# Performance work log

Measured on AMD Instinct MI355X. Metric: run time of the kernel, lower is better.

The kernel has to match this reference:

```python
import jax, jax.numpy as jnp
from jax import lax
import numpy as np

NUM_SCALES = 4
NUM_ORI = 8
SIGMA = 2.0
FILTER_SIZE = 32  # min(512 // 2**scale, 32) == 32 for all scales, already even
J = 4
POOL = 2 ** J  # 16


def _make_gabor_filters():
    """Replicates GaborWavelet2D + _init_wavelet_filters. Returns (real, imag) stacks
    of shape [num_scales*num_ori, 1, FILTER_SIZE, FILTER_SIZE]."""
    oris = np.linspace(0.0, np.pi, NUM_ORI)
    idx = np.arange(FILTER_SIZE, dtype=np.float32) - FILTER_SIZE // 2
    X, Y = np.meshgrid(idx, idx, indexing='ij')
    reals, imags = [], []
    for scale in range(1, NUM_SCALES + 1):
        for o in oris:
            Xr = X * np.cos(o) + Y * np.sin(o)
            Yr = -X * np.sin(o) + Y * np.cos(o)
            sf = scale * SIGMA
            env = np.exp(-0.5 * (Xr ** 2 + Yr ** 2) / sf ** 2)
            phase = 2.0 * np.pi * (1.0 / scale) * Xr / sf
            reals.append(env * np.cos(phase))
            imags.append(env * np.sin(phase))
    real = np.stack(reals).astype(np.float32)[:, None]  # [32,1,32,32]
    imag = np.stack(imags).astype(np.float32)[:, None]
    return real, imag


def setup_inputs() -> dict:
    key = jax.random.key(0)
    x = jax.random.normal(key, (8, 3, 512, 512), dtype=jnp.float32)
    w_real, w_imag = _make_gabor_filters()
    return {"x": x, "w_real": jnp.asarray(w_real), "w_imag": jnp.asarray(w_imag)}


def _avg_pool(t):
    # torch F.avg_pool2d(kernel=16), default stride=kernel, floor mode (drop remainder)
    B, C, H, W = t.shape
    Ho, Wo = H // POOL, W // POOL
    t = t[:, :, :Ho * POOL, :Wo * POOL]
    return t.reshape(B, C, Ho, POOL, Wo, POOL).mean(axis=(3, 5))


def reference(x, w_real, w_imag):
    # x: [B,3,512,512]
    x_gray = x.mean(axis=1, keepdims=True)  # [B,1,H,W]
    S0 = _avg_pool(x_gray)  # [B,1,32,32]

    pad = FILTER_SIZE // 2  # 16 -> conv output is (H+1, W+1) = 513x513
    w = jnp.concatenate([w_real, w_imag], axis=0)  # [64,1,32,32]
    conv = lax.conv_general_dilated(
        x_gray, w, window_strides=(1, 1), padding=((pad, pad), (pad, pad)),
        dimension_numbers=('NCHW', 'OIHW', 'NCHW'))  # [B,64,513,513], cross-correlation like torch
    nf = w_real.shape[0]
    cr, ci = conv[:, :nf], conv[:, nf:]
    mag = jnp.sqrt(cr ** 2 + ci ** 2 + 1e-8)  # [B,32,513,513]
    S1 = _avg_pool(mag)  # [B,32,32,32]
    return (S0, S1)
```

## Files before the change

### kernel.cpp

```cpp
#include <hip/hip_runtime.h>
#include <math.h>

#define IMG   512
#define NFILT 32
#define NPAIR 16
#define PI_F  3.14159265358979323846f
#define GS    104

typedef _Float16 v8h __attribute__((ext_vector_type(8)));
typedef float    v4f __attribute__((ext_vector_type(4)));

__device__ __forceinline__ unsigned pkrtz(float a, float b) {
    typedef __fp16 f16x2 __attribute__((ext_vector_type(2)));
    union { f16x2 h; unsigned u; } x;
    x.h = __builtin_amdgcn_cvt_pkrtz(a, b);
    return x.u;
}

template <int CTRL>
__device__ __forceinline__ float dpp_add(float v) {
    int t = __builtin_amdgcn_update_dpp(0, __float_as_int(v), CTRL, 0xf, 0xf, true);
    return v + __int_as_float(t);
}

__device__ __forceinline__ float xor32_add(float m) {
    float a = m, b = m;
    asm("v_permlane32_swap_b32 %0, %1" : "+v"(a), "+v"(b));
    return a + b;
}

#if __has_builtin(__builtin_amdgcn_sqrtf)
__device__ __forceinline__ float fsqrt(float x) { return __builtin_amdgcn_sqrtf(x); }
#else
__device__ __forceinline__ float fsqrt(float x) { return sqrtf(x); }
#endif

__device__ __forceinline__ void bar_lgkm() {
    asm volatile("s_waitcnt lgkmcnt(0)\n\ts_barrier" ::: "memory");
}

__device__ __forceinline__ v8h ldfrag(const uint4* p) {
    union { uint4 u; v8h h; } x; x.u = *p; return x.h;
}

__global__ void make_tables(unsigned* __restrict__ tabs) {
    __shared__ _Float16 P[5][168];
    const int fo = blockIdx.x;
    const int tid = threadIdx.x;
    for (int e = tid; e < 5 * 168; e += 256) ((_Float16*)P)[e] = (_Float16)0.0f;
    __syncthreads();
    if (tid < 160) {
        int tbl = tid >> 5, t = tid & 31;
        int s = (fo >> 3) + 1, o = fo & 7;
        float theta = (float)o * (PI_F / 7.0f);
        float sf = (float)s * 2.0f;
        float kf = 2.0f * PI_F / ((float)s * sf);
        float a = kf * cosf(theta), b = kf * sinf(theta);
        float d = (float)(t - 16);
        float env = expf(-0.5f * d * d / (sf * sf));
        float v;
        switch (tbl) {
            case 0: v =  env * cosf(b * d); break;
            case 1: v =  env * sinf(b * d); break;
            case 2: v =  env * cosf(a * d); break;
            case 3: v =  env * sinf(a * d); break;
            default: v = -env * sinf(a * d); break;
        }
        P[tbl][t + 64] = (_Float16)v;
    }
    __syncthreads();
    unsigned* dst = tabs + (size_t)fo * 3200;
    for (int e = tid; e < 3200; e += 256) {
        int tbl  = e / 640;  int rem2 = e - tbl * 640;
        int copy = rem2 / 80; int idw = rem2 - copy * 80;
        int p0 = (idw >> 2) * 8 + copy + (idw & 3) * 2;
        union { unsigned u; _Float16 h[2]; } p;
        p.h[0] = P[tbl][p0];
        p.h[1] = P[tbl][p0 + 1];
        dst[e] = p.u;
    }
}

__launch_bounds__(512, 4)
__global__ void conv_kernel(const float* __restrict__ x,
                            const uint4* __restrict__ tabs,
                            float* __restrict__ s0out,
                            float* __restrict__ s1out) {
    __shared__ _Float16 gray[96 * GS];
    __shared__ _Float16 Tre[2][64 * GS];
    __shared__ _Float16 Tim[2][64 * GS];
    __shared__ float    s1st[NFILT * 16];

    const int bx = blockIdx.x;
    const int n  = bx >> 6;
    const int t6 = bx & 63;
    const int ty = t6 >> 3, tx = t6 & 7;
    const int r0g = ty * 64 - 16;
    const int c0g = tx * 64 - 16;
    const int tid = threadIdx.x;

    const int lane = tid & 63;
    const int w    = tid >> 6;
    const int r4   = w & 3;
    const int half = w >> 2;
    const int nn   = lane & 15;
    const int q8   = (lane >> 4) << 3;
    const int q4   = (lane >> 4) << 2;
    const int cr   = r4 * 16 + nn;
    const int u    = q8 - cr + 64;
    const int b0   = r4 >> 1;
    const int uoff = (u & 7) * 20 + (u >> 3);

    const uint4* fb0 = tabs + uoff;
    v8h Gre0[2], Gim0[2], Fre[2], Fim[2];
    #pragma unroll
    for (int j = 0; j < 2; ++j) {
        int idx = (b0 + j) * 4;
        Gre0[j] = ldfrag(fb0 + idx);
        Gim0[j] = ldfrag(fb0 + 160 + idx);
        Fre[j]  = ldfrag(fb0 + 320 + idx);
        Fim[j]  = ldfrag(fb0 + 480 + idx);
    }

    {
        const float* c0p = x + (size_t)n * 3 * IMG * IMG;
        const float* c1p = c0p + IMG * IMG;
        const float* c2p = c0p + 2 * IMG * IMG;
        for (int e = tid; e < 96 * 24; e += 512) {
            int hr = e / 24, g4 = e - hr * 24;
            int hc0 = g4 * 4;
            int gr = r0g + hr, gc0 = c0g + hc0;
            float4 v = make_float4(0.f, 0.f, 0.f, 0.f);
            if (hr < 95 && (unsigned)gr < IMG && (unsigned)gc0 < IMG) {
                size_t off = ((size_t)gr * IMG + gc0) >> 2;
                float4 a = ((const float4*)c0p)[off];
                float4 b = ((const float4*)c1p)[off];
                float4 c = ((const float4*)c2p)[off];
                v.x = (a.x + b.x + c.x) * (1.0f / 3.0f);
                v.y = (a.y + b.y + c.y) * (1.0f / 3.0f);
                v.z = (a.z + b.z + c.z) * (1.0f / 3.0f);
                v.w = (hc0 == 92) ? 0.0f : (a.w + b.w + c.w) * (1.0f / 3.0f);
            }
            uint2 w2;
            w2.x = pkrtz(v.x, v.y);
            w2.y = pkrtz(v.z, v.w);
            *(uint2*)(&gray[hr * GS + hc0]) = w2;
        }
    }
    __syncthreads();

    if (tid < 256) {
        int cell = tid >> 4, sub = tid & 15;
        int pr = cell >> 2, pc = cell & 3;
        const _Float16* row = &gray[(16 + pr * 16 + sub) * GS + 16 + pc * 16];
        float s = 0.0f;
        #pragma unroll
        for (int j = 0; j < 16; ++j) s += (float)row[j];
        s += __shfl_xor(s, 1);
        s += __shfl_xor(s, 2);
        s += __shfl_xor(s, 4);
        s += __shfl_xor(s, 8);
        if (sub == 0)
            s0out[(size_t)n * 1024 + (ty * 4 + pr) * 32 + (tx * 4 + pc)] = s * (1.0f / 256.0f);
    }


    v8h Agray[3][2];
    #pragma unroll
    for (int mi = 0; mi < 3; ++mi)
        #pragma unroll
        for (int j = 0; j < 2; ++j)
            Agray[mi][j] = *(const v8h*)(&gray[((half * 3 + mi) * 16 + nn) * GS + (b0 + j) * 32 + q8]);

    #pragma unroll
    for (int mi = 0; mi < 3; ++mi) {
        int mt = half * 3 + mi;
        v4f aR = {0.f, 0.f, 0.f, 0.f}, aI = {0.f, 0.f, 0.f, 0.f};
        #pragma unroll
        for (int j = 0; j < 2; ++j) {
            aR = __builtin_amdgcn_mfma_f32_16x16x32_f16(Agray[mi][j], Gre0[j], aR, 0, 0, 0);
            aI = __builtin_amdgcn_mfma_f32_16x16x32_f16(Agray[mi][j], Gim0[j], aI, 0, 0, 0);
        }
        int mb = mt * 16 + q4;
        uint2 pr, pi;
        pr.x = pkrtz(aR[0], aR[1]);  pr.y = pkrtz(aR[2], aR[3]);
        pi.x = pkrtz(aI[0], aI[1]);  pi.y = pkrtz(aI[2], aI[3]);
        *(uint2*)(&Tre[0][cr * GS + mb]) = pr;
        *(uint2*)(&Tim[0][cr * GS + mb]) = pi;
    }
    __syncthreads();

    for (int p = 0; p < NPAIR; ++p) {
        const _Float16* Tr  = Tre[p & 1];
        const _Float16* Ti  = Tim[p & 1];
        _Float16*       Trn = Tre[(p + 1) & 1];
        _Float16*       Tin = Tim[(p + 1) & 1];
        const int fa  = ((p >> 2) << 3) + (p & 3);
        const int fbi = ((p >> 2) << 3) + 7 - (p & 3);
        const int nxp = (p < NPAIR - 1) ? p + 1 : p;
        const int nxfa = ((nxp >> 2) << 3) + (nxp & 3);
        const uint4* fbn = tabs + (size_t)nxfa * 800 + uoff;

        v8h Gre[2], Gim[2];
        #pragma unroll
        for (int j = 0; j < 2; ++j) {
            int idx = (b0 + j) * 4;
            Gre[j] = ldfrag(fbn + idx);
            Gim[j] = ldfrag(fbn + 160 + idx);
        }

        #pragma unroll
        for (int ni = 0; ni < 2; ++ni) {
            int nt = half * 2 + ni;
            v4f P1 = {0.f, 0.f, 0.f, 0.f}, P2 = {0.f, 0.f, 0.f, 0.f};
            v4f P3 = {0.f, 0.f, 0.f, 0.f}, P4 = {0.f, 0.f, 0.f, 0.f};
            #pragma unroll
            for (int j = 0; j < 2; ++j) {
                v8h tR = *(const v8h*)(&Tr[(nt * 16 + nn) * GS + (b0 + j) * 32 + q8]);
                v8h tI = *(const v8h*)(&Ti[(nt * 16 + nn) * GS + (b0 + j) * 32 + q8]);
                P1 = __builtin_amdgcn_mfma_f32_16x16x32_f16(Fre[j], tR, P1, 0, 0, 0);
                P2 = __builtin_amdgcn_mfma_f32_16x16x32_f16(Fim[j], tI, P2, 0, 0, 0);
                P3 = __builtin_amdgcn_mfma_f32_16x16x32_f16(Fre[j], tI, P3, 0, 0, 0);
                P4 = __builtin_amdgcn_mfma_f32_16x16x32_f16(Fim[j], tR, P4, 0, 0, 0);
            }
            v4f are = P1 - P2, aim = P3 + P4;
            v4f bre = P1 + P2, bim = P3 - P4;
            float sa0 = fsqrt(fmaf(are[0], are[0], fmaf(aim[0], aim[0], 1e-8f)));
            float sa1 = fsqrt(fmaf(are[1], are[1], fmaf(aim[1], aim[1], 1e-8f)));
            float sa2 = fsqrt(fmaf(are[2], are[2], fmaf(aim[2], aim[2], 1e-8f)));
            float sa3 = fsqrt(fmaf(are[3], are[3], fmaf(aim[3], aim[3], 1e-8f)));
            float sb0 = fsqrt(fmaf(bre[0], bre[0], fmaf(bim[0], bim[0], 1e-8f)));
            float sb1 = fsqrt(fmaf(bre[1], bre[1], fmaf(bim[1], bim[1], 1e-8f)));
            float sb2 = fsqrt(fmaf(bre[2], bre[2], fmaf(bim[2], bim[2], 1e-8f)));
            float sb3 = fsqrt(fmaf(bre[3], bre[3], fmaf(bim[3], bim[3], 1e-8f)));
            float ma = (sa0 + sa1) + (sa2 + sa3);
            float mb = (sb0 + sb1) + (sb2 + sb3);
            ma = dpp_add<0xB1>(ma);   mb = dpp_add<0xB1>(mb);
            ma = dpp_add<0x4E>(ma);   mb = dpp_add<0x4E>(mb);
            ma = dpp_add<0x141>(ma);  mb = dpp_add<0x141>(mb);
            ma = dpp_add<0x140>(ma);  mb = dpp_add<0x140>(mb);
            ma += __shfl_xor(ma, 16); mb += __shfl_xor(mb, 16);
            ma = xor32_add(ma);       mb = xor32_add(mb);
            if (lane == 0) {
                s1st[fa  * 16 + r4 * 4 + nt] = ma;
                s1st[fbi * 16 + r4 * 4 + nt] = mb;
            }
        }

        if (p < NPAIR - 1) {
            #pragma unroll
            for (int mi = 0; mi < 3; ++mi) {
                int mt = half * 3 + mi;
                v4f aR = {0.f, 0.f, 0.f, 0.f}, aI = {0.f, 0.f, 0.f, 0.f};
                #pragma unroll
                for (int j = 0; j < 2; ++j) {
                    aR = __builtin_amdgcn_mfma_f32_16x16x32_f16(Agray[mi][j], Gre[j], aR, 0, 0, 0);
                    aI = __builtin_amdgcn_mfma_f32_16x16x32_f16(Agray[mi][j], Gim[j], aI, 0, 0, 0);
                }
                int mb = mt * 16 + q4;
                uint2 pr, pi;
                pr.x = pkrtz(aR[0], aR[1]);  pr.y = pkrtz(aR[2], aR[3]);
                pi.x = pkrtz(aI[0], aI[1]);  pi.y = pkrtz(aI[2], aI[3]);
                *(uint2*)(&Trn[cr * GS + mb]) = pr;
                *(uint2*)(&Tin[cr * GS + mb]) = pi;
            }
            #pragma unroll
            for (int j = 0; j < 2; ++j) {
                int idx = (b0 + j) * 4;
                Fre[j] = ldfrag(fbn + 320 + idx);
                Fim[j] = ldfrag(fbn + 480 + idx);
            }
        }
        bar_lgkm();
    }

    float* s1b = s1out + (size_t)n * NFILT * 32 * 32;
    for (int e = tid; e < NFILT * 16; e += 512) {
        int fi = e >> 4, cell = e & 15;
        int r4c = cell >> 2, ntc = cell & 3;
        s1b[((size_t)fi * 32 + (ty * 4 + r4c)) * 32 + (tx * 4 + ntc)] =
            s1st[e] * (1.0f / 256.0f);
    }
}

extern "C" void kernel_launch(void* const* d_in, const int* in_sizes, int n_in,
                              void* d_out, int out_size, void* d_ws, size_t ws_size,
                              hipStream_t stream) {
    const float* x = (const float*)d_in[0];
    float* out = (float*)d_out;
    unsigned* tabs = (unsigned*)d_ws;

    hipLaunchKernelGGL(make_tables, dim3(32), dim3(256), 0, stream, tabs);
    hipLaunchKernelGGL(conv_kernel, dim3(512), dim3(512), 0, stream,
                       x, (const uint4*)tabs, out, out + 8192);
}
```

Measured before the change: 113.3 us.

## Software-pipeline magnitude reduction one pair behind MFMA accumulation

Defers the sqrt and wavefront-reduction epilogue for each filter pair to the next loop iteration, so it interleaves with that iteration's MFMA work. Both column tiles' accumulators are computed together, and s_setprio raises wave priority around the matrix-core section. The cross-lane swap is replaced by a generic shuffle xor 32. This holds more accumulators live, which raises register pressure and adds an extra epilogue and barrier after the loop. The final deferred reduction uses filter indices 27 and 28, which matches p=15.

```diff
diff --git a/kernel.cpp b/kernel.cpp
--- a/kernel.cpp
+++ b/kernel.cpp
@@ -23,11 +23,6 @@
     return v + __int_as_float(t);
 }
 
-__device__ __forceinline__ float xor32_add(float m) {
-    float a = m, b = m;
-    asm("v_permlane32_swap_b32 %0, %1" : "+v"(a), "+v"(b));
-    return a + b;
-}
 
 #if __has_builtin(__builtin_amdgcn_sqrtf)
 __device__ __forceinline__ float fsqrt(float x) { return __builtin_amdgcn_sqrtf(x); }
@@ -164,7 +159,6 @@
             s0out[(size_t)n * 1024 + (ty * 4 + pr) * 32 + (tx * 4 + pc)] = s * (1.0f / 256.0f);
     }
 
-
     v8h Agray[3][2];
     #pragma unroll
     for (int mi = 0; mi < 3; ++mi)
@@ -190,60 +184,80 @@
     }
     __syncthreads();
 
+    auto magred = [&](v4f P1, v4f P2, v4f P3, v4f P4, int faI, int fbI, int ntc) {
+        v4f are = P1 - P2, aim = P3 + P4;
+        v4f bre = P1 + P2, bim = P3 - P4;
+        float sa0 = fsqrt(fmaf(are[0], are[0], fmaf(aim[0], aim[0], 1e-8f)));
+        float sa1 = fsqrt(fmaf(are[1], are[1], fmaf(aim[1], aim[1], 1e-8f)));
+        float sa2 = fsqrt(fmaf(are[2], are[2], fmaf(aim[2], aim[2], 1e-8f)));
+        float sa3 = fsqrt(fmaf(are[3], are[3], fmaf(aim[3], aim[3], 1e-8f)));
+        float sb0 = fsqrt(fmaf(bre[0], bre[0], fmaf(bim[0], bim[0], 1e-8f)));
+        float sb1 = fsqrt(fmaf(bre[1], bre[1], fmaf(bim[1], bim[1], 1e-8f)));
+        float sb2 = fsqrt(fmaf(bre[2], bre[2], fmaf(bim[2], bim[2], 1e-8f)));
+        float sb3 = fsqrt(fmaf(bre[3], bre[3], fmaf(bim[3], bim[3], 1e-8f)));
+        float ma = (sa0 + sa1) + (sa2 + sa3);
+        float mb = (sb0 + sb1) + (sb2 + sb3);
+        ma = dpp_add<0xB1>(ma);   mb = dpp_add<0xB1>(mb);
+        ma = dpp_add<0x4E>(ma);   mb = dpp_add<0x4E>(mb);
+        ma = dpp_add<0x141>(ma);  mb = dpp_add<0x141>(mb);
+        ma = dpp_add<0x140>(ma);  mb = dpp_add<0x140>(mb);
+        ma += __shfl_xor(ma, 16); mb += __shfl_xor(mb, 16);
+        ma += __shfl_xor(ma, 32); mb += __shfl_xor(mb, 32);
+        if (lane == 0) {
+            s1st[faI * 16 + r4 * 4 + ntc] = ma;
+            s1st[fbI * 16 + r4 * 4 + ntc] = mb;
+        }
+    };
+
+    v4f P1a = {0,0,0,0}, P2a = {0,0,0,0}, P3a = {0,0,0,0}, P4a = {0,0,0,0};
+    v4f P1b = {0,0,0,0}, P2b = {0,0,0,0}, P3b = {0,0,0,0}, P4b = {0,0,0,0};
+
     for (int p = 0; p < NPAIR; ++p) {
         const _Float16* Tr  = Tre[p & 1];
         const _Float16* Ti  = Tim[p & 1];
         _Float16*       Trn = Tre[(p + 1) & 1];
         _Float16*       Tin = Tim[(p + 1) & 1];
-        const int fa  = ((p >> 2) << 3) + (p & 3);
-        const int fbi = ((p >> 2) << 3) + 7 - (p & 3);
-        const int nxp = (p < NPAIR - 1) ? p + 1 : p;
+        const int nxp  = (p < NPAIR - 1) ? p + 1 : p;
         const int nxfa = ((nxp >> 2) << 3) + (nxp & 3);
         const uint4* fbn = tabs + (size_t)nxfa * 800 + uoff;
 
         v8h Gre[2], Gim[2];
-        #pragma unroll
-        for (int j = 0; j < 2; ++j) {
-            int idx = (b0 + j) * 4;
-            Gre[j] = ldfrag(fbn + idx);
-            Gim[j] = ldfrag(fbn + 160 + idx);
-        }
-
-        #pragma unroll
-        for (int ni = 0; ni < 2; ++ni) {
-            int nt = half * 2 + ni;
-            v4f P1 = {0.f, 0.f, 0.f, 0.f}, P2 = {0.f, 0.f, 0.f, 0.f};
-            v4f P3 = {0.f, 0.f, 0.f, 0.f}, P4 = {0.f, 0.f, 0.f, 0.f};
+        if (p < NPAIR - 1) {
             #pragma unroll
             for (int j = 0; j < 2; ++j) {
-                v8h tR = *(const v8h*)(&Tr[(nt * 16 + nn) * GS + (b0 + j) * 32 + q8]);
-                v8h tI = *(const v8h*)(&Ti[(nt * 16 + nn) * GS + (b0 + j) * 32 + q8]);
-                P1 = __builtin_amdgcn_mfma_f32_16x16x32_f16(Fre[j], tR, P1, 0, 0, 0);
-                P2 = __builtin_amdgcn_mfma_f32_16x16x32_f16(Fim[j], tI, P2, 0, 0, 0);
-                P3 = __builtin_amdgcn_mfma_f32_16x16x32_f16(Fre[j], tI, P3, 0, 0, 0);
-                P4 = __builtin_amdgcn_mfma_f32_16x16x32_f16(Fim[j], tR, P4, 0, 0, 0);
-            }
-            v4f are = P1 - P2, aim = P3 + P4;
-            v4f bre = P1 + P2, bim = P3 - P4;
-            float sa0 = fsqrt(fmaf(are[0], are[0], fmaf(aim[0], aim[0], 1e-8f)));
-            float sa1 = fsqrt(fmaf(are[1], are[1], fmaf(aim[1], aim[1], 1e-8f)));
-            float sa2 = fsqrt(fmaf(are[2], are[2], fmaf(aim[2], aim[2], 1e-8f)));
-            float sa3 = fsqrt(fmaf(are[3], are[3], fmaf(aim[3], aim[3], 1e-8f)));
-            float sb0 = fsqrt(fmaf(bre[0], bre[0], fmaf(bim[0], bim[0], 1e-8f)));
-            float sb1 = fsqrt(fmaf(bre[1], bre[1], fmaf(bim[1], bim[1], 1e-8f)));
-            float sb2 = fsqrt(fmaf(bre[2], bre[2], fmaf(bim[2], bim[2], 1e-8f)));
-            float sb3 = fsqrt(fmaf(bre[3], bre[3], fmaf(bim[3], bim[3], 1e-8f)));
-            float ma = (sa0 + sa1) + (sa2 + sa3);
-            float mb = (sb0 + sb1) + (sb2 + sb3);
-            ma = dpp_add<0xB1>(ma);   mb = dpp_add<0xB1>(mb);
-            ma = dpp_add<0x4E>(ma);   mb = dpp_add<0x4E>(mb);
-            ma = dpp_add<0x141>(ma);  mb = dpp_add<0x141>(mb);
-            ma = dpp_add<0x140>(ma);  mb = dpp_add<0x140>(mb);
-            ma += __shfl_xor(ma, 16); mb += __shfl_xor(mb, 16);
-            ma = xor32_add(ma);       mb = xor32_add(mb);
-            if (lane == 0) {
-                s1st[fa  * 16 + r4 * 4 + nt] = ma;
-                s1st[fbi * 16 + r4 * 4 + nt] = mb;
+                int idx = (b0 + j) * 4;
+                Gre[j] = ldfrag(fbn + idx);
+                Gim[j] = ldfrag(fbn + 160 + idx);
+            }
+        }
+
+        if (p > 0) {
+            const int q    = p - 1;
+            const int pfa  = ((q >> 2) << 3) + (q & 3);
+            const int pfbi = ((q >> 2) << 3) + 7 - (q & 3);
+            magred(P1a, P2a, P3a, P4a, pfa, pfbi, half * 2 + 0);
+            magred(P1b, P2b, P3b, P4b, pfa, pfbi, half * 2 + 1);
+        }
+
+        __builtin_amdgcn_s_setprio(1);
+        {
+            int nt0 = half * 2 + 0, nt1 = half * 2 + 1;
+            P1a = {0,0,0,0}; P2a = {0,0,0,0}; P3a = {0,0,0,0}; P4a = {0,0,0,0};
+            P1b = {0,0,0,0}; P2b = {0,0,0,0}; P3b = {0,0,0,0}; P4b = {0,0,0,0};
+            #pragma unroll
+            for (int j = 0; j < 2; ++j) {
+                v8h tR0 = *(const v8h*)(&Tr[(nt0 * 16 + nn) * GS + (b0 + j) * 32 + q8]);
+                v8h tI0 = *(const v8h*)(&Ti[(nt0 * 16 + nn) * GS + (b0 + j) * 32 + q8]);
+                v8h tR1 = *(const v8h*)(&Tr[(nt1 * 16 + nn) * GS + (b0 + j) * 32 + q8]);
+                v8h tI1 = *(const v8h*)(&Ti[(nt1 * 16 + nn) * GS + (b0 + j) * 32 + q8]);
+                P1a = __builtin_amdgcn_mfma_f32_16x16x32_f16(Fre[j], tR0, P1a, 0, 0, 0);
+                P2a = __builtin_amdgcn_mfma_f32_16x16x32_f16(Fim[j], tI0, P2a, 0, 0, 0);
+                P3a = __builtin_amdgcn_mfma_f32_16x16x32_f16(Fre[j], tI0, P3a, 0, 0, 0);
+                P4a = __builtin_amdgcn_mfma_f32_16x16x32_f16(Fim[j], tR0, P4a, 0, 0, 0);
+                P1b = __builtin_amdgcn_mfma_f32_16x16x32_f16(Fre[j], tR1, P1b, 0, 0, 0);
+                P2b = __builtin_amdgcn_mfma_f32_16x16x32_f16(Fim[j], tI1, P2b, 0, 0, 0);
+                P3b = __builtin_amdgcn_mfma_f32_16x16x32_f16(Fre[j], tI1, P3b, 0, 0, 0);
+                P4b = __builtin_amdgcn_mfma_f32_16x16x32_f16(Fim[j], tR1, P4b, 0, 0, 0);
             }
         }
 
@@ -264,15 +278,22 @@
                 *(uint2*)(&Trn[cr * GS + mb]) = pr;
                 *(uint2*)(&Tin[cr * GS + mb]) = pi;
             }
+            __builtin_amdgcn_s_setprio(0);
             #pragma unroll
             for (int j = 0; j < 2; ++j) {
                 int idx = (b0 + j) * 4;
                 Fre[j] = ldfrag(fbn + 320 + idx);
                 Fim[j] = ldfrag(fbn + 480 + idx);
             }
+        } else {
+            __builtin_amdgcn_s_setprio(0);
         }
         bar_lgkm();
     }
+
+    magred(P1a, P2a, P3a, P4a, 27, 28, half * 2 + 0);
+    magred(P1b, P2b, P3b, P4b, 27, 28, half * 2 + 1);
+    __syncthreads();
 
     float* s1b = s1out + (size_t)n * NFILT * 32 * 32;
     for (int e = tid; e < NFILT * 16; e += 512) {
```

Result: slower. 115.7 us (+2.1%).

## Keep separable-conv intermediate in registers, drop LDS double buffer and barriers

Applied to the files above, without the earlier changes.

Restructures the two-stage separable Gabor convolution so each wave computes its first-stage (row) MFMA output directly into register fragments. Those fragments are packed to fp16 and fed straight into 16x16x16 MFMAs for the second stage, removing the shared-memory T buffers, per-filter barriers and the staging array for S1. S1 results are written directly to global memory from each wave. The cost is redundant first-stage work: each wave recomputes the row convolution for its own tile, doubling those MFMAs, and filter fragments are reloaded from global memory every iteration.

```diff
diff --git a/kernel.cpp b/kernel.cpp
--- a/kernel.cpp
+++ b/kernel.cpp
@@ -8,7 +8,26 @@
 #define GS    104
 
 typedef _Float16 v8h __attribute__((ext_vector_type(8)));
+typedef _Float16 v4h __attribute__((ext_vector_type(4)));
 typedef float    v4f __attribute__((ext_vector_type(4)));
+
+#define MF32(a, b, c) __builtin_amdgcn_mfma_f32_16x16x32_f16((a), (b), (c), 0, 0, 0)
+
+#if __has_builtin(__builtin_amdgcn_mfma_f32_16x16x16f16)
+__device__ __forceinline__ v4f mf16(v4h a, v4h b, v4f c) {
+    return __builtin_amdgcn_mfma_f32_16x16x16f16(a, b, c, 0, 0, 0);
+}
+#elif __has_builtin(__builtin_amdgcn_mfma_f32_16x16x16_f16)
+__device__ __forceinline__ v4f mf16(v4h a, v4h b, v4f c) {
+    return __builtin_amdgcn_mfma_f32_16x16x16_f16(a, b, c, 0, 0, 0);
+}
+#else
+__device__ __forceinline__ v4f mf16(v4h a, v4h b, v4f c) {
+    asm("v_mfma_f32_16x16x16_f16 %0, %1, %2, %0" : "+v"(c) : "v"(a), "v"(b));
+    return c;
+}
+#endif
+#define MF16(a, b, c) mf16((a), (b), (c))
 
 __device__ __forceinline__ unsigned pkrtz(float a, float b) {
     typedef __fp16 f16x2 __attribute__((ext_vector_type(2)));
@@ -23,24 +42,23 @@
     return v + __int_as_float(t);
 }
 
-__device__ __forceinline__ float xor32_add(float m) {
-    float a = m, b = m;
-    asm("v_permlane32_swap_b32 %0, %1" : "+v"(a), "+v"(b));
-    return a + b;
-}
-
 #if __has_builtin(__builtin_amdgcn_sqrtf)
 __device__ __forceinline__ float fsqrt(float x) { return __builtin_amdgcn_sqrtf(x); }
 #else
 __device__ __forceinline__ float fsqrt(float x) { return sqrtf(x); }
 #endif
 
-__device__ __forceinline__ void bar_lgkm() {
-    asm volatile("s_waitcnt lgkmcnt(0)\n\ts_barrier" ::: "memory");
-}
-
 __device__ __forceinline__ v8h ldfrag(const uint4* p) {
     union { uint4 u; v8h h; } x; x.u = *p; return x.h;
+}
+__device__ __forceinline__ v4h ldfrag2(const uint2* p) {
+    union { uint2 u; v4h h; } x; x.u = *p; return x.h;
+}
+__device__ __forceinline__ v4h pk4(v4f a) {
+    union { unsigned u[2]; v4h h; } x;
+    x.u[0] = pkrtz(a[0], a[1]);
+    x.u[1] = pkrtz(a[2], a[3]);
+    return x.h;
 }
 
 __global__ void make_tables(unsigned* __restrict__ tabs) {
@@ -87,9 +105,6 @@
                             float* __restrict__ s0out,
                             float* __restrict__ s1out) {
     __shared__ _Float16 gray[96 * GS];
-    __shared__ _Float16 Tre[2][64 * GS];
-    __shared__ _Float16 Tim[2][64 * GS];
-    __shared__ float    s1st[NFILT * 16];
 
     const int bx = blockIdx.x;
     const int n  = bx >> 6;
@@ -102,25 +117,20 @@
     const int lane = tid & 63;
     const int w    = tid >> 6;
     const int r4   = w & 3;
-    const int half = w >> 2;
+    const int hh   = w >> 2;
     const int nn   = lane & 15;
     const int q8   = (lane >> 4) << 3;
     const int q4   = (lane >> 4) << 2;
-    const int cr   = r4 * 16 + nn;
-    const int u    = q8 - cr + 64;
     const int b0   = r4 >> 1;
-    const int uoff = (u & 7) * 20 + (u >> 3);
-
-    const uint4* fb0 = tabs + uoff;
-    v8h Gre0[2], Gim0[2], Fre[2], Fim[2];
-    #pragma unroll
-    for (int j = 0; j < 2; ++j) {
-        int idx = (b0 + j) * 4;
-        Gre0[j] = ldfrag(fb0 + idx);
-        Gim0[j] = ldfrag(fb0 + 160 + idx);
-        Fre[j]  = ldfrag(fb0 + 320 + idx);
-        Fim[j]  = ldfrag(fb0 + 480 + idx);
-    }
+
+    const int rr   = r4 * 16 + nn;
+    const int u0F  = q4 - rr + 64;
+    const int offF = (u0F & 7) * 20 + (u0F >> 3);
+    const int cG0  = 2 * hh * 16 + nn;
+    const int uG0  = q8 - cG0 + 64;
+    const int uG1  = uG0 - 16;
+    const int offG0 = (uG0 & 7) * 20 + (uG0 >> 3);
+    const int offG1 = (uG1 & 7) * 20 + (uG1 >> 3);
 
     {
         const float* c0p = x + (size_t)n * 3 * IMG * IMG;
@@ -164,122 +174,114 @@
             s0out[(size_t)n * 1024 + (ty * 4 + pr) * 32 + (tx * 4 + pc)] = s * (1.0f / 256.0f);
     }
 
-
-    v8h Agray[3][2];
+    v8h Agray[4][2];
     #pragma unroll
-    for (int mi = 0; mi < 3; ++mi)
-        #pragma unroll
-        for (int j = 0; j < 2; ++j)
-            Agray[mi][j] = *(const v8h*)(&gray[((half * 3 + mi) * 16 + nn) * GS + (b0 + j) * 32 + q8]);
-
-    #pragma unroll
-    for (int mi = 0; mi < 3; ++mi) {
-        int mt = half * 3 + mi;
-        v4f aR = {0.f, 0.f, 0.f, 0.f}, aI = {0.f, 0.f, 0.f, 0.f};
-        #pragma unroll
-        for (int j = 0; j < 2; ++j) {
-            aR = __builtin_amdgcn_mfma_f32_16x16x32_f16(Agray[mi][j], Gre0[j], aR, 0, 0, 0);
-            aI = __builtin_amdgcn_mfma_f32_16x16x32_f16(Agray[mi][j], Gim0[j], aI, 0, 0, 0);
-        }
-        int mb = mt * 16 + q4;
-        uint2 pr, pi;
-        pr.x = pkrtz(aR[0], aR[1]);  pr.y = pkrtz(aR[2], aR[3]);
-        pi.x = pkrtz(aI[0], aI[1]);  pi.y = pkrtz(aI[2], aI[3]);
-        *(uint2*)(&Tre[0][cr * GS + mb]) = pr;
-        *(uint2*)(&Tim[0][cr * GS + mb]) = pi;
-    }
-    __syncthreads();
+    for (int mi = 0; mi < 4; ++mi)
+        #pragma unroll
+        for (int jj = 0; jj < 2; ++jj)
+            Agray[mi][jj] = *(const v8h*)(&gray[((2 * b0 + mi) * 16 + nn) * GS + (hh + jj) * 32 + q8]);
+
+    float* s1b = s1out + (size_t)n * NFILT * 1024;
+
+    auto magstore = [&](v4f P1, v4f P2, v4f P3, v4f P4, int faI, int fbI, int ct) {
+        v4f are = P1 - P2, aim = P3 + P4;
+        v4f bre = P1 + P2, bim = P3 - P4;
+        float sa0 = fsqrt(fmaf(are[0], are[0], fmaf(aim[0], aim[0], 1e-8f)));
+        float sa1 = fsqrt(fmaf(are[1], are[1], fmaf(aim[1], aim[1], 1e-8f)));
+        float sa2 = fsqrt(fmaf(are[2], are[2], fmaf(aim[2], aim[2], 1e-8f)));
+        float sa3 = fsqrt(fmaf(are[3], are[3], fmaf(aim[3], aim[3], 1e-8f)));
+        float sb0 = fsqrt(fmaf(bre[0], bre[0], fmaf(bim[0], bim[0], 1e-8f)));
+        float sb1 = fsqrt(fmaf(bre[1], bre[1], fmaf(bim[1], bim[1], 1e-8f)));
+        float sb2 = fsqrt(fmaf(bre[2], bre[2], fmaf(bim[2], bim[2], 1e-8f)));
+        float sb3 = fsqrt(fmaf(bre[3], bre[3], fmaf(bim[3], bim[3], 1e-8f)));
+        float ma = (sa0 + sa1) + (sa2 + sa3);
+        float mb = (sb0 + sb1) + (sb2 + sb3);
+        ma = dpp_add<0xB1>(ma);   mb = dpp_add<0xB1>(mb);
+        ma = dpp_add<0x4E>(ma);   mb = dpp_add<0x4E>(mb);
+        ma = dpp_add<0x141>(ma);  mb = dpp_add<0x141>(mb);
+        ma = dpp_add<0x140>(ma);  mb = dpp_add<0x140>(mb);
+        ma += __shfl_xor(ma, 16); mb += __shfl_xor(mb, 16);
+        ma += __shfl_xor(ma, 32); mb += __shfl_xor(mb, 32);
+        if (lane == 0) {
+            s1b[((size_t)faI * 32 + (ty * 4 + r4)) * 32 + (tx * 4 + ct)] = ma * (1.0f / 256.0f);
+            s1b[((size_t)fbI * 32 + (ty * 4 + r4)) * 32 + (tx * 4 + ct)] = mb * (1.0f / 256.0f);
+        }
+    };
 
     for (int p = 0; p < NPAIR; ++p) {
-        const _Float16* Tr  = Tre[p & 1];
-        const _Float16* Ti  = Tim[p & 1];
-        _Float16*       Trn = Tre[(p + 1) & 1];
-        _Float16*       Tin = Tim[(p + 1) & 1];
         const int fa  = ((p >> 2) << 3) + (p & 3);
         const int fbi = ((p >> 2) << 3) + 7 - (p & 3);
-        const int nxp = (p < NPAIR - 1) ? p + 1 : p;
-        const int nxfa = ((nxp >> 2) << 3) + (nxp & 3);
-        const uint4* fbn = tabs + (size_t)nxfa * 800 + uoff;
-
-        v8h Gre[2], Gim[2];
-        #pragma unroll
-        for (int j = 0; j < 2; ++j) {
-            int idx = (b0 + j) * 4;
-            Gre[j] = ldfrag(fbn + idx);
-            Gim[j] = ldfrag(fbn + 160 + idx);
-        }
-
-        #pragma unroll
-        for (int ni = 0; ni < 2; ++ni) {
-            int nt = half * 2 + ni;
-            v4f P1 = {0.f, 0.f, 0.f, 0.f}, P2 = {0.f, 0.f, 0.f, 0.f};
-            v4f P3 = {0.f, 0.f, 0.f, 0.f}, P4 = {0.f, 0.f, 0.f, 0.f};
+        const uint4* ft  = tabs + (size_t)fa * 800;
+        const uint2* ft2 = (const uint2*)ft;
+
+        v4h Fr[4], Fi[4];
+        #pragma unroll
+        for (int s = 0; s < 4; ++s) {
+            Fr[s] = ldfrag2(ft2 + 640 + 2 * offF + 8 * b0 + 4 * s);
+            Fi[s] = ldfrag2(ft2 + 960 + 2 * offF + 8 * b0 + 4 * s);
+        }
+        v8h Gr[2], Gi[2];
+        #pragma unroll
+        for (int jj = 0; jj < 2; ++jj) {
+            Gr[jj] = ldfrag(ft + offG0 + (hh + jj) * 4);
+            Gi[jj] = ldfrag(ft + 160 + offG0 + (hh + jj) * 4);
+        }
+
+        v4h tre[4], tim[4];
+        #pragma unroll
+        for (int mi = 0; mi < 4; ++mi) {
+            v4f aR = {0.f, 0.f, 0.f, 0.f}, aI = {0.f, 0.f, 0.f, 0.f};
+            aR = MF32(Agray[mi][0], Gr[0], aR);
+            aI = MF32(Agray[mi][0], Gi[0], aI);
+            aR = MF32(Agray[mi][1], Gr[1], aR);
+            aI = MF32(Agray[mi][1], Gi[1], aI);
+            tre[mi] = pk4(aR);
+            tim[mi] = pk4(aI);
+        }
+
+        v8h Gr1[2], Gi1[2];
+        #pragma unroll
+        for (int jj = 0; jj < 2; ++jj) {
+            Gr1[jj] = ldfrag(ft + offG1 + (hh + jj) * 4);
+            Gi1[jj] = ldfrag(ft + 160 + offG1 + (hh + jj) * 4);
+        }
+
+        {
+            v4f P1 = {0.f,0.f,0.f,0.f}, P2 = {0.f,0.f,0.f,0.f};
+            v4f P3 = {0.f,0.f,0.f,0.f}, P4 = {0.f,0.f,0.f,0.f};
             #pragma unroll
-            for (int j = 0; j < 2; ++j) {
-                v8h tR = *(const v8h*)(&Tr[(nt * 16 + nn) * GS + (b0 + j) * 32 + q8]);
-                v8h tI = *(const v8h*)(&Ti[(nt * 16 + nn) * GS + (b0 + j) * 32 + q8]);
-                P1 = __builtin_amdgcn_mfma_f32_16x16x32_f16(Fre[j], tR, P1, 0, 0, 0);
-                P2 = __builtin_amdgcn_mfma_f32_16x16x32_f16(Fim[j], tI, P2, 0, 0, 0);
-                P3 = __builtin_amdgcn_mfma_f32_16x16x32_f16(Fre[j], tI, P3, 0, 0, 0);
-                P4 = __builtin_amdgcn_mfma_f32_16x16x32_f16(Fim[j], tR, P4, 0, 0, 0);
+            for (int s = 0; s < 4; ++s) {
+                P1 = MF16(Fr[s], tre[s], P1);
+                P2 = MF16(Fi[s], tim[s], P2);
+                P3 = MF16(Fr[s], tim[s], P3);
+                P4 = MF16(Fi[s], tre[s], P4);
             }
-            v4f are = P1 - P2, aim = P3 + P4;
-            v4f bre = P1 + P2, bim = P3 - P4;
-            float sa0 = fsqrt(fmaf(are[0], are[0], fmaf(aim[0], aim[0], 1e-8f)));
-            float sa1 = fsqrt(fmaf(are[1], are[1], fmaf(aim[1], aim[1], 1e-8f)));
-            float sa2 = fsqrt(fmaf(are[2], are[2], fmaf(aim[2], aim[2], 1e-8f)));
-            float sa3 = fsqrt(fmaf(are[3], are[3], fmaf(aim[3], aim[3], 1e-8f)));
-            float sb0 = fsqrt(fmaf(bre[0], bre[0], fmaf(bim[0], bim[0], 1e-8f)));
-            float sb1 = fsqrt(fmaf(bre[1], bre[1], fmaf(bim[1], bim[1], 1e-8f)));
-            float sb2 = fsqrt(fmaf(bre[2], bre[2], fmaf(bim[2], bim[2], 1e-8f)));
-            float sb3 = fsqrt(fmaf(bre[3], bre[3], fmaf(bim[3], bim[3], 1e-8f)));
-            float ma = (sa0 + sa1) + (sa2 + sa3);
-            float mb = (sb0 + sb1) + (sb2 + sb3);
-            ma = dpp_add<0xB1>(ma);   mb = dpp_add<0xB1>(mb);
-            ma = dpp_add<0x4E>(ma);   mb = dpp_add<0x4E>(mb);
-            ma = dpp_add<0x141>(ma);  mb = dpp_add<0x141>(mb);
-            ma = dpp_add<0x140>(ma);  mb = dpp_add<0x140>(mb);
-            ma += __shfl_xor(ma, 16); mb += __shfl_xor(mb, 16);
-            ma = xor32_add(ma);       mb = xor32_add(mb);
-            if (lane == 0) {
-                s1st[fa  * 16 + r4 * 4 + nt] = ma;
-                s1st[fbi * 16 + r4 * 4 + nt] = mb;
+            magstore(P1, P2, P3, P4, fa, fbi, 2 * hh);
+        }
+
+        #pragma unroll
+        for (int mi = 0; mi < 4; ++mi) {
+            v4f aR = {0.f, 0.f, 0.f, 0.f}, aI = {0.f, 0.f, 0.f, 0.f};
+            aR = MF32(Agray[mi][0], Gr1[0], aR);
+            aI = MF32(Agray[mi][0], Gi1[0], aI);
+            aR = MF32(Agray[mi][1], Gr1[1], aR);
+            aI = MF32(Agray[mi][1], Gi1[1], aI);
+            tre[mi] = pk4(aR);
+            tim[mi] = pk4(aI);
+        }
+
+        {
+            v4f P1 = {0.f,0.f,0.f,0.f}, P2 = {0.f,0.f,0.f,0.f};
+            v4f P3 = {0.f,0.f,0.f,0.f}, P4 = {0.f,0.f,0.f,0.f};
+            #pragma unroll
+            for (int s = 0; s < 4; ++s) {
+                P1 = MF16(Fr[s], tre[s], P1);
+                P2 = MF16(Fi[s], tim[s], P2);
+                P3 = MF16(Fr[s], tim[s], P3);
+                P4 = MF16(Fi[s], tre[s], P4);
             }
-        }
-
-        if (p < NPAIR - 1) {
-            #pragma unroll
-            for (int mi = 0; mi < 3; ++mi) {
-                int mt = half * 3 + mi;
-                v4f aR = {0.f, 0.f, 0.f, 0.f}, aI = {0.f, 0.f, 0.f, 0.f};
-                #pragma unroll
-                for (int j = 0; j < 2; ++j) {
-                    aR = __builtin_amdgcn_mfma_f32_16x16x32_f16(Agray[mi][j], Gre[j], aR, 0, 0, 0);
-                    aI = __builtin_amdgcn_mfma_f32_16x16x32_f16(Agray[mi][j], Gim[j], aI, 0, 0, 0);
-                }
-                int mb = mt * 16 + q4;
-                uint2 pr, pi;
-                pr.x = pkrtz(aR[0], aR[1]);  pr.y = pkrtz(aR[2], aR[3]);
-                pi.x = pkrtz(aI[0], aI[1]);  pi.y = pkrtz(aI[2], aI[3]);
-                *(uint2*)(&Trn[cr * GS + mb]) = pr;
-                *(uint2*)(&Tin[cr * GS + mb]) = pi;
-            }
-            #pragma unroll
-            for (int j = 0; j < 2; ++j) {
-                int idx = (b0 + j) * 4;
-                Fre[j] = ldfrag(fbn + 320 + idx);
-                Fim[j] = ldfrag(fbn + 480 + idx);
-            }
-        }
-        bar_lgkm();
-    }
-
-    float* s1b = s1out + (size_t)n * NFILT * 32 * 32;
-    for (int e = tid; e < NFILT * 16; e += 512) {
-        int fi = e >> 4, cell = e & 15;
-        int r4c = cell >> 2, ntc = cell & 3;
-        s1b[((size_t)fi * 32 + (ty * 4 + r4c)) * 32 + (tx * 4 + ntc)] =
-            s1st[e] * (1.0f / 256.0f);
+            magstore(P1, P2, P3, P4, fa, fbi, 2 * hh + 1);
+        }
     }
 }
 
```

Result: slower. 144.1 us (+27.1%).

## Split filter pairs across two blocks per tile and alias gray into T buffers

Applied to the files above, without the earlier changes.

Each 64x64 tile is now processed by two blocks, each handling 8 of the 16 filter pairs, doubling the grid to 1024 blocks so more blocks are in flight across the CUs. The gray buffer is aliased into the unified LDS area used for the double-buffered T tiles, and the s1 staging buffer is removed with results written straight to global memory, which cuts LDS per block and raises launch bounds to 6. The cost is that gray loading, channel averaging and the first separable pass are repeated in both blocks, and an extra barrier is needed before the aliased buffer is overwritten.

```diff
diff --git a/kernel.cpp b/kernel.cpp
--- a/kernel.cpp
+++ b/kernel.cpp
@@ -3,9 +3,9 @@
 
 #define IMG   512
 #define NFILT 32
-#define NPAIR 16
 #define PI_F  3.14159265358979323846f
 #define GS    104
+#define TBUF  (64 * GS)
 
 typedef _Float16 v8h __attribute__((ext_vector_type(8)));
 typedef float    v4f __attribute__((ext_vector_type(4)));
@@ -21,12 +21,6 @@
 __device__ __forceinline__ float dpp_add(float v) {
     int t = __builtin_amdgcn_update_dpp(0, __float_as_int(v), CTRL, 0xf, 0xf, true);
     return v + __int_as_float(t);
-}
-
-__device__ __forceinline__ float xor32_add(float m) {
-    float a = m, b = m;
-    asm("v_permlane32_swap_b32 %0, %1" : "+v"(a), "+v"(b));
-    return a + b;
 }
 
 #if __has_builtin(__builtin_amdgcn_sqrtf)
@@ -81,23 +75,24 @@
     }
 }
 
-__launch_bounds__(512, 4)
+__launch_bounds__(512, 6)
 __global__ void conv_kernel(const float* __restrict__ x,
                             const uint4* __restrict__ tabs,
                             float* __restrict__ s0out,
                             float* __restrict__ s1out) {
-    __shared__ _Float16 gray[96 * GS];
-    __shared__ _Float16 Tre[2][64 * GS];
-    __shared__ _Float16 Tim[2][64 * GS];
-    __shared__ float    s1st[NFILT * 16];
+    __shared__ _Float16 U[4 * TBUF];
+    _Float16* gray = U;
 
     const int bx = blockIdx.x;
-    const int n  = bx >> 6;
-    const int t6 = bx & 63;
+    const int n   = bx >> 7;
+    const int rem = bx & 127;
+    const int t6  = rem >> 1;
+    const int fs  = rem & 1;
     const int ty = t6 >> 3, tx = t6 & 7;
     const int r0g = ty * 64 - 16;
     const int c0g = tx * 64 - 16;
     const int tid = threadIdx.x;
+    const int P0 = fs * 8;
 
     const int lane = tid & 63;
     const int w    = tid >> 6;
@@ -111,7 +106,8 @@
     const int b0   = r4 >> 1;
     const int uoff = (u & 7) * 20 + (u >> 3);
 
-    const uint4* fb0 = tabs + uoff;
+    const int fa0 = ((P0 >> 2) << 3) + (P0 & 3);
+    const uint4* fb0 = tabs + (size_t)fa0 * 800 + uoff;
     v8h Gre0[2], Gim0[2], Fre[2], Fim[2];
     #pragma unroll
     for (int j = 0; j < 2; ++j) {
@@ -149,7 +145,7 @@
     }
     __syncthreads();
 
-    if (tid < 256) {
+    if (fs == 0 && tid < 256) {
         int cell = tid >> 4, sub = tid & 15;
         int pr = cell >> 2, pc = cell & 3;
         const _Float16* row = &gray[(16 + pr * 16 + sub) * GS + 16 + pc * 16];
@@ -164,13 +160,14 @@
             s0out[(size_t)n * 1024 + (ty * 4 + pr) * 32 + (tx * 4 + pc)] = s * (1.0f / 256.0f);
     }
 
-
     v8h Agray[3][2];
     #pragma unroll
     for (int mi = 0; mi < 3; ++mi)
         #pragma unroll
         for (int j = 0; j < 2; ++j)
             Agray[mi][j] = *(const v8h*)(&gray[((half * 3 + mi) * 16 + nn) * GS + (b0 + j) * 32 + q8]);
+
+    bar_lgkm();
 
     #pragma unroll
     for (int mi = 0; mi < 3; ++mi) {
@@ -185,19 +182,21 @@
         uint2 pr, pi;
         pr.x = pkrtz(aR[0], aR[1]);  pr.y = pkrtz(aR[2], aR[3]);
         pi.x = pkrtz(aI[0], aI[1]);  pi.y = pkrtz(aI[2], aI[3]);
-        *(uint2*)(&Tre[0][cr * GS + mb]) = pr;
-        *(uint2*)(&Tim[0][cr * GS + mb]) = pi;
-    }
-    __syncthreads();
-
-    for (int p = 0; p < NPAIR; ++p) {
-        const _Float16* Tr  = Tre[p & 1];
-        const _Float16* Ti  = Tim[p & 1];
-        _Float16*       Trn = Tre[(p + 1) & 1];
-        _Float16*       Tin = Tim[(p + 1) & 1];
+        *(uint2*)(&U[cr * GS + mb]) = pr;
+        *(uint2*)(&U[TBUF + cr * GS + mb]) = pi;
+    }
+    bar_lgkm();
+
+    float* s1b = s1out + (size_t)n * NFILT * 1024;
+
+    for (int p = P0; p < P0 + 8; ++p) {
+        _Float16* Trc = U + (size_t)(p & 1) * (2 * TBUF);
+        _Float16* Tic = Trc + TBUF;
+        _Float16* Trn = U + (size_t)((p + 1) & 1) * (2 * TBUF);
+        _Float16* Tin = Trn + TBUF;
         const int fa  = ((p >> 2) << 3) + (p & 3);
         const int fbi = ((p >> 2) << 3) + 7 - (p & 3);
-        const int nxp = (p < NPAIR - 1) ? p + 1 : p;
+        const int nxp = (p < P0 + 7) ? p + 1 : p;
         const int nxfa = ((nxp >> 2) << 3) + (nxp & 3);
         const uint4* fbn = tabs + (size_t)nxfa * 800 + uoff;
 
@@ -216,8 +215,8 @@
             v4f P3 = {0.f, 0.f, 0.f, 0.f}, P4 = {0.f, 0.f, 0.f, 0.f};
             #pragma unroll
             for (int j = 0; j < 2; ++j) {
-                v8h tR = *(const v8h*)(&Tr[(nt * 16 + nn) * GS + (b0 + j) * 32 + q8]);
-                v8h tI = *(const v8h*)(&Ti[(nt * 16 + nn) * GS + (b0 + j) * 32 + q8]);
+                v8h tR = *(const v8h*)(&Trc[(nt * 16 + nn) * GS + (b0 + j) * 32 + q8]);
+                v8h tI = *(const v8h*)(&Tic[(nt * 16 + nn) * GS + (b0 + j) * 32 + q8]);
                 P1 = __builtin_amdgcn_mfma_f32_16x16x32_f16(Fre[j], tR, P1, 0, 0, 0);
                 P2 = __builtin_amdgcn_mfma_f32_16x16x32_f16(Fim[j], tI, P2, 0, 0, 0);
                 P3 = __builtin_amdgcn_mfma_f32_16x16x32_f16(Fre[j], tI, P3, 0, 0, 0);
@@ -240,14 +239,14 @@
             ma = dpp_add<0x141>(ma);  mb = dpp_add<0x141>(mb);
             ma = dpp_add<0x140>(ma);  mb = dpp_add<0x140>(mb);
             ma += __shfl_xor(ma, 16); mb += __shfl_xor(mb, 16);
-            ma = xor32_add(ma);       mb = xor32_add(mb);
+            ma += __shfl_xor(ma, 32); mb += __shfl_xor(mb, 32);
             if (lane == 0) {
-                s1st[fa  * 16 + r4 * 4 + nt] = ma;
-                s1st[fbi * 16 + r4 * 4 + nt] = mb;
-            }
-        }
-
-        if (p < NPAIR - 1) {
+                s1b[((size_t)fa  * 32 + (ty * 4 + r4)) * 32 + (tx * 4 + nt)] = ma * (1.0f / 256.0f);
+                s1b[((size_t)fbi * 32 + (ty * 4 + r4)) * 32 + (tx * 4 + nt)] = mb * (1.0f / 256.0f);
+            }
+        }
+
+        if (p < P0 + 7) {
             #pragma unroll
             for (int mi = 0; mi < 3; ++mi) {
                 int mt = half * 3 + mi;
@@ -273,14 +272,6 @@
         }
         bar_lgkm();
     }
-
-    float* s1b = s1out + (size_t)n * NFILT * 32 * 32;
-    for (int e = tid; e < NFILT * 16; e += 512) {
-        int fi = e >> 4, cell = e & 15;
-        int r4c = cell >> 2, ntc = cell & 3;
-        s1b[((size_t)fi * 32 + (ty * 4 + r4c)) * 32 + (tx * 4 + ntc)] =
-            s1st[e] * (1.0f / 256.0f);
-    }
 }
 
 extern "C" void kernel_launch(void* const* d_in, const int* in_sizes, int n_in,
@@ -291,6 +282,6 @@
     unsigned* tabs = (unsigned*)d_ws;
 
     hipLaunchKernelGGL(make_tables, dim3(32), dim3(256), 0, stream, tabs);
-    hipLaunchKernelGGL(conv_kernel, dim3(512), dim3(512), 0, stream,
+    hipLaunchKernelGGL(conv_kernel, dim3(1024), dim3(512), 0, stream,
                        x, (const uint4*)tabs, out, out + 8192);
 }
```

Result: slower. 171.9 us (+51.8%).
